# Performance work log

Measured on AMD Instinct MI355X. Metric: run time of the kernel, lower is better.

The kernel has to match this reference:

```python
import jax, jax.numpy as jnp
import numpy as np

EPS = 1e-5
H, W, D_FULL, D_RFFT, DIM = 9, 11, 9, 5, 900  # spectral grid 9x11x9, rfft last dim -> 5

def layer_norm(x, gamma, beta):
    mu = jnp.mean(x, axis=-1, keepdims=True)
    var = jnp.var(x, axis=-1, keepdims=True)
    return (x - mu) * jax.lax.rsqrt(var + EPS) * gamma + beta

def setup_inputs() -> dict:
    key = jax.random.key(0)
    ks = jax.random.split(key, 12)
    B, N, C = 64, H * W * D_FULL, DIM  # N = 891
    hidden, rank = int(C * 2.0), C // 2  # 1800, 450
    return {
        "x": jax.random.normal(ks[0], (B, N, C), dtype=jnp.float32),
        # Global_Filter complex weight: (h, w, d, dim, 2), init ~ N(0,1)*0.02
        "cw": jax.random.normal(ks[1], (H, W, D_RFFT, C, 2), dtype=jnp.float32) * 0.02,
        "gamma1": jnp.ones((C,), jnp.float32),
        "beta1": jnp.zeros((C,), jnp.float32),
        "gamma2": jnp.ones((C,), jnp.float32),
        "beta2": jnp.zeros((C,), jnp.float32),
        # low-rank MLP (torch Linear weights are (out, in); we apply x @ W.T)
        "u1_w": jax.random.normal(ks[2], (rank, C), jnp.float32) * (1.0 / np.sqrt(C)),
        "v1_w": jax.random.normal(ks[3], (hidden, rank), jnp.float32) * (1.0 / np.sqrt(rank)),
        "v1_b": jnp.zeros((hidden,), jnp.float32),
        "u2_w": jax.random.normal(ks[4], (rank, hidden), jnp.float32) * (1.0 / np.sqrt(hidden)),
        "v2_w": jax.random.normal(ks[5], (C, rank), jnp.float32) * (1.0 / np.sqrt(rank)),
        "v2_b": jnp.zeros((C,), jnp.float32),
    }

def reference(x, cw, gamma1, beta1, gamma2, beta2, u1_w, v1_w, v1_b, u2_w, v2_w, v2_b):
    B, N, C = x.shape
    # norm1 -> global spectral filter
    y = layer_norm(x, gamma1, beta1)
    y = y.reshape(B, H, W, D_FULL, C)
    yf = jnp.fft.rfftn(y, axes=(1, 2, 3), norm="ortho")  # (B, 9, 11, 5, C) complex
    weight = jax.lax.complex(cw[..., 0], cw[..., 1])      # (9, 11, 5, C)
    yf = yf * weight
    y = jnp.fft.irfftn(yf, s=(H, W, D_FULL), axes=(1, 2, 3), norm="ortho")
    y = y.reshape(B, N, C)
    # norm2 -> low-rank MLP (dropout/droppath = identity in eval)
    z = layer_norm(y, gamma2, beta2)
    z = jnp.einsum("bnc,rc->bnr", z, u1_w)
    z = jnp.einsum("bnr,hr->bnh", z, v1_w) + v1_b
    z = jax.nn.gelu(z, approximate=False)
    z = jnp.einsum("bnh,rh->bnr", z, u2_w)
    z = jnp.einsum("bnr,cr->bnc", z, v2_w) + v2_b
    return x + z
```

## Files before the change

### kernel.cpp

```cpp
#include <hip/hip_runtime.h>


typedef unsigned short u16;
typedef __bf16 bf16x8 __attribute__((ext_vector_type(8)));
typedef float f32x4 __attribute__((ext_vector_type(4)));

#define LN_EPS 1e-5f
#define CH 16

constexpr float KC9[9] = {
  1.0f, 0.766044443118978f, 0.17364817766693041f, -0.4999999999999998f,
  -0.9396926207859083f, -0.9396926207859084f, -0.5000000000000004f,
  0.17364817766692997f, 0.7660444431189778f };
constexpr float KS9[9] = {
  0.0f, 0.6427876096865393f, 0.984807753012208f, 0.8660254037844387f,
  0.3420201433256689f, -0.34202014332566866f, -0.8660254037844385f,
  -0.9848077530122081f, -0.6427876096865396f };
constexpr float KC11[11] = {
  1.0f, 0.8412535328311812f, 0.41541501300188644f, -0.14231483827328512f,
  -0.654860733945285f, -0.9594929736144974f, -0.9594929736144974f,
  -0.6548607339452852f, -0.14231483827328543f, 0.4154150130018863f,
  0.8412535328311811f };
constexpr float KS11[11] = {
  0.0f, 0.5406408174555976f, 0.9096319953545183f, 0.9898214418809327f,
  0.7557495743542583f, 0.2817325568414297f, -0.2817325568414296f,
  -0.7557495743542582f, -0.9898214418809327f, -0.9096319953545184f,
  -0.5406408174555979f };

__device__ __forceinline__ u16 f2bf(float f) {
  unsigned int u = __float_as_uint(f);
  return (u16)((u + 0x7fffu + ((u >> 16) & 1u)) >> 16);
}
__device__ __forceinline__ float gelu_f(float v) {
  float t = 0.7978845608028654f * v * (1.f + 0.044715f * v * v);
  float e = __expf(2.f * t);
  float th = 1.f - 2.f * __builtin_amdgcn_rcpf(e + 1.f);
  return 0.5f * v * (1.f + th);
}

__global__ __launch_bounds__(256) void k_cvt(const float* __restrict__ s, u16* __restrict__ d,
                                             int rows, int sc, int dc,
                                             const float* __restrict__ gamma) {
  int i = blockIdx.x * 256 + threadIdx.x;
  if (i >= rows * dc) return;
  int r = i / dc, c = i % dc;
  u16 o = 0;
  if (c < sc) {
    float v = s[(size_t)r * sc + c];
    if (gamma) v *= gamma[c];
    o = f2bf(v);
  }
  d[i] = o;
}

__global__ __launch_bounds__(256) void k_bias1(const float* __restrict__ u1w,
                                               const float* __restrict__ b2,
                                               float* __restrict__ out) {
  int r = blockIdx.x * 256 + threadIdx.x;
  if (r < 450) {
    float s = 0.f;
    for (int c = 0; c < 900; c++) s += u1w[r * 900 + c] * b2[c];
    out[r] = s;
  }
}

__global__ __launch_bounds__(256) void k_stats1(const float* __restrict__ x,
                                                float2* __restrict__ stats) {
  int tok = blockIdx.x * 4 + (threadIdx.x >> 6);
  int l = threadIdx.x & 63;
  const float* row = x + (size_t)tok * 900;
  float s1 = 0.f, s2 = 0.f;
#pragma unroll
  for (int j = 0; j < 15; j++) {
    int c = l + j * 64;
    if (c < 900) { float a = row[c]; s1 += a; s2 += a * a; }
  }
#pragma unroll
  for (int off = 32; off; off >>= 1) { s1 += __shfl_xor(s1, off, 64); s2 += __shfl_xor(s2, off, 64); }
  if (l == 0) {
    float m = s1 * (1.f / 900.f);
    float var = s2 * (1.f / 900.f) - m * m;
    stats[tok] = make_float2(m, rsqrtf(var + LN_EPS));
  }
}

__global__ __launch_bounds__(256) void k_spectral(const float* __restrict__ x,
                                                  const float2* __restrict__ stats,
                                                  const float* __restrict__ g1,
                                                  const float* __restrict__ b1,
                                                  const float* __restrict__ cw,
                                                  float* __restrict__ y) {
  __shared__ float sre[5 * 99 * CH];
  __shared__ float sim[5 * 99 * CH];
  int b = blockIdx.x / 57, cc = blockIdx.x % 57;
  int c0 = cc * CH;
  int t = threadIdx.x;
  const float* xb = x + (size_t)b * 801900;
  const float2* st = stats + (size_t)b * 891;

  for (int col = t; col < 99 * CH; col += 256) {
    int pos = col / CH, c = col % CH;
    int cg = c0 + c; bool ok = cg < 900;
    float g = ok ? g1[cg] : 0.f, be = ok ? b1[cg] : 0.f;
    float yv[9];
#pragma unroll
    for (int d = 0; d < 9; d++) {
      float a = ok ? xb[(size_t)(pos * 9 + d) * 900 + cg] : 0.f;
      float2 s = st[pos * 9 + d];
      yv[d] = (a - s.x) * s.y * g + be;
    }
#pragma unroll
    for (int kd = 0; kd < 5; kd++) {
      float re = 0.f, im = 0.f;
#pragma unroll
      for (int d = 0; d < 9; d++) { int j = (kd * d) % 9; re += yv[d] * KC9[j]; im -= yv[d] * KS9[j]; }
      sre[(kd * 99 + pos) * CH + c] = re;
      sim[(kd * 99 + pos) * CH + c] = im;
    }
  }
  __syncthreads();

  for (int col = t; col < 5 * 9 * CH; col += 256) {
    int kd = col / (9 * CH), r = col % (9 * CH), h = r / CH, c = r % CH;
    int base = (kd * 99 + h * 11) * CH + c;
    float xr[11], xi[11];
#pragma unroll
    for (int w = 0; w < 11; w++) { xr[w] = sre[base + w * CH]; xi[w] = sim[base + w * CH]; }
#pragma unroll
    for (int k = 0; k < 11; k++) {
      float yr = 0.f, yi = 0.f;
#pragma unroll
      for (int w = 0; w < 11; w++) {
        int j = (k * w) % 11; float cf = KC11[j], sf = KS11[j];
        yr += xr[w] * cf + xi[w] * sf;
        yi += xi[w] * cf - xr[w] * sf;
      }
      sre[base + k * CH] = yr; sim[base + k * CH] = yi;
    }
  }
  __syncthreads();

  for (int col = t; col < 5 * 11 * CH; col += 256) {
    int kd = col / (11 * CH), r = col % (11 * CH), kw = r / CH, c = r % CH;
    int cg = c0 + c;
    int base = (kd * 99 + kw) * CH + c;
    float xr[9], xi[9];
#pragma unroll
    for (int h = 0; h < 9; h++) { xr[h] = sre[base + h * 11 * CH]; xi[h] = sim[base + h * 11 * CH]; }
    float zr[9], zi[9];
#pragma unroll
    for (int k = 0; k < 9; k++) {
      float yr = 0.f, yi = 0.f;
#pragma unroll
      for (int h = 0; h < 9; h++) {
        int j = (k * h) % 9; float cf = KC9[j], sf = KS9[j];
        yr += xr[h] * cf + xi[h] * sf;
        yi += xi[h] * cf - xr[h] * sf;
      }
      float wr = 0.f, wi = 0.f;
      if (cg < 900) {
        size_t widx = ((size_t)((k * 11 + kw) * 5 + kd) * 900 + cg) * 2;
        wr = cw[widx]; wi = cw[widx + 1];
      }
      zr[k] = yr * wr - yi * wi;
      zi[k] = yr * wi + yi * wr;
    }
#pragma unroll
    for (int h = 0; h < 9; h++) {
      float orr = 0.f, oi = 0.f;
#pragma unroll
      for (int k = 0; k < 9; k++) {
        int j = (k * h) % 9; float cf = KC9[j], sf = KS9[j];
        orr += zr[k] * cf - zi[k] * sf;
        oi  += zi[k] * cf + zr[k] * sf;
      }
      sre[base + h * 11 * CH] = orr; sim[base + h * 11 * CH] = oi;
    }
  }
  __syncthreads();

  for (int col = t; col < 5 * 9 * CH; col += 256) {
    int kd = col / (9 * CH), r = col % (9 * CH), h = r / CH, c = r % CH;
    int base = (kd * 99 + h * 11) * CH + c;
    float xr[11], xi[11];
#pragma unroll
    for (int w = 0; w < 11; w++) { xr[w] = sre[base + w * CH]; xi[w] = sim[base + w * CH]; }
#pragma unroll
    for (int k = 0; k < 11; k++) {
      float yr = 0.f, yi = 0.f;
#pragma unroll
      for (int w = 0; w < 11; w++) {
        int j = (k * w) % 11; float cf = KC11[j], sf = KS11[j];
        yr += xr[w] * cf - xi[w] * sf;
        yi += xi[w] * cf + xr[w] * sf;
      }
      sre[base + k * CH] = yr; sim[base + k * CH] = yi;
    }
  }
  __syncthreads();

  for (int col = t; col < 99 * CH; col += 256) {
    int pos = col / CH, c = col % CH;
    int cg = c0 + c;
    if (cg >= 900) continue;
    float Xr[5], Xi[5];
#pragma unroll
    for (int k = 0; k < 5; k++) { Xr[k] = sre[(k * 99 + pos) * CH + c]; Xi[k] = sim[(k * 99 + pos) * CH + c]; }
#pragma unroll
    for (int d = 0; d < 9; d++) {
      float acc = Xr[0];
#pragma unroll
      for (int k = 1; k < 5; k++) { int j = (k * d) % 9; acc += 2.f * (Xr[k] * KC9[j] - Xi[k] * KS9[j]); }
      y[((size_t)b * 891 + pos * 9 + d) * 900 + cg] = acc * (1.f / 891.f);
    }
  }
}

__global__ __launch_bounds__(256) void k_ln2(const float* __restrict__ y, u16* __restrict__ yn) {
  int tok = blockIdx.x * 4 + (threadIdx.x >> 6);
  int l = threadIdx.x & 63;
  const float* row = y + (size_t)tok * 900;
  float v[15];
  float s1 = 0.f, s2 = 0.f;
#pragma unroll
  for (int j = 0; j < 15; j++) {
    int c = l + j * 64;
    float a = (c < 900) ? row[c] : 0.f;
    v[j] = a; s1 += a; s2 += a * a;
  }
#pragma unroll
  for (int off = 32; off; off >>= 1) { s1 += __shfl_xor(s1, off, 64); s2 += __shfl_xor(s2, off, 64); }
  float m = s1 * (1.f / 900.f);
  float var = s2 * (1.f / 900.f) - m * m;
  float rs = rsqrtf(var + LN_EPS);
  u16* orow = yn + (size_t)tok * 928;
#pragma unroll
  for (int j = 0; j < 15; j++) {
    int c = l + j * 64;
    if (c < 900) orow[c] = f2bf((v[j] - m) * rs);
    else if (c < 928) orow[c] = 0;
  }
}

typedef __attribute__((address_space(1))) void gvoid;
typedef __attribute__((address_space(3))) void svoid;

__device__ __forceinline__ void stage16(const u16* g, u16* lbase, int lane) {
#if __has_builtin(__builtin_amdgcn_global_load_lds)
  __builtin_amdgcn_global_load_lds((gvoid*)(void*)g, (svoid*)lbase, 16, 0, 0);
#else
  *(uint4*)(lbase + lane * 8) = *(const uint4*)g;
#endif
}

template <int EPI>
__global__ __launch_bounds__(256, 2) void k_gemm(
    const u16* __restrict__ A, const u16* __restrict__ B,
    int M, int N, int Kt, int ldk, int NT,
    u16* __restrict__ Ob, int ldo, int Nstore,
    const float* __restrict__ bias,
    const float* __restrict__ Xres, float* __restrict__ Of) {
  __shared__ u16 As[128 * 32];
  __shared__ u16 Bs[128 * 32];
  int t = threadIdx.x, w = t >> 6, l = t & 63;
  int mt = blockIdx.x / NT, nt = blockIdx.x % NT;
  int m0 = mt * 128, n0 = nt * 128;
  int arow = (w << 4) + (l >> 2);
  int koff = (l & 3) * 8;
  int wm = (w >> 1) << 6, wn = (w & 1) << 6;
  int fr = l & 15, fq = l >> 4;

  f32x4 acc[4][4];
  f32x4 zero = {0.f, 0.f, 0.f, 0.f};
#pragma unroll
  for (int i = 0; i < 4; i++)
#pragma unroll
    for (int j = 0; j < 4; j++) acc[i][j] = zero;

  for (int kt = 0; kt < Kt; ++kt) {
    int k0 = kt * 32;
#pragma unroll
    for (int j = 0; j < 2; j++) {
      int r = (j << 6) + arow;
      int gm = m0 + r; gm = gm < M ? gm : M - 1;
      stage16(A + (size_t)gm * ldk + (k0 + koff), &As[((j << 6) + (w << 4)) * 32], l);
      int gn = n0 + r; gn = gn < N ? gn : N - 1;
      stage16(B + (size_t)gn * ldk + (k0 + koff), &Bs[((j << 6) + (w << 4)) * 32], l);
    }
    __syncthreads();
    bf16x8 af[4], bfr[4];
#pragma unroll
    for (int i = 0; i < 4; i++) af[i] = *(const bf16x8*)&As[(wm + (i << 4) + fr) * 32 + fq * 8];
#pragma unroll
    for (int i = 0; i < 4; i++) bfr[i] = *(const bf16x8*)&Bs[(wn + (i << 4) + fr) * 32 + fq * 8];
#pragma unroll
    for (int i = 0; i < 4; i++)
#pragma unroll
      for (int j = 0; j < 4; j++)
        acc[i][j] = __builtin_amdgcn_mfma_f32_16x16x32_bf16(af[i], bfr[j], acc[i][j], 0, 0, 0);
    __syncthreads();
  }

#pragma unroll
  for (int j = 0; j < 4; j++) {
    int gn = n0 + wn + (j << 4) + fr;
    float bv = 0.f;
    if (EPI != 2) bv = (gn < Nstore) ? bias[gn] : 0.f;
#pragma unroll
    for (int i = 0; i < 4; i++) {
#pragma unroll
      for (int r = 0; r < 4; r++) {
        int gm = m0 + wm + (i << 4) + (fq << 2) + r;
        if (gm < M) {
          float val = acc[i][j][r] + bv;
          if (EPI == 1) val = gelu_f(val);
          if (EPI == 3) {
            if (gn < Nstore) Of[(size_t)gm * Nstore + gn] = val + Xres[(size_t)gm * Nstore + gn];
          } else {
            if (gn < ldo) Ob[(size_t)gm * ldo + gn] = (gn < Nstore) ? f2bf(val) : (u16)0;
          }
        }
      }
    }
  }
}

extern "C" void kernel_launch(void* const* d_in, const int* in_sizes, int n_in,
                              void* d_out, int out_size, void* d_ws, size_t ws_size,
                              hipStream_t stream) {
  const float* x   = (const float*)d_in[0];
  const float* cw  = (const float*)d_in[1];
  const float* g1  = (const float*)d_in[2];
  const float* b1  = (const float*)d_in[3];
  const float* g2  = (const float*)d_in[4];
  const float* b2  = (const float*)d_in[5];
  const float* u1w = (const float*)d_in[6];
  const float* v1w = (const float*)d_in[7];
  const float* v1b = (const float*)d_in[8];
  const float* u2w = (const float*)d_in[9];
  const float* v2w = (const float*)d_in[10];
  const float* v2b = (const float*)d_in[11];

  char* ws = (char*)d_ws;
  float* y   = (float*)ws;
  u16*   t2  = (u16*)ws;
  u16*   t3  = (u16*)(ws + 228096000);
  u16*   u1g = (u16*)(ws + 286488576);
  u16*   v1c = (u16*)(ws + 287323776);
  u16*   u2c = (u16*)(ws + 289166976);
  u16*   v2c = (u16*)(ws + 290808576);
  float* b1r = (float*)(ws + 291730176);

  u16*    yn    = (u16*)d_out;
  u16*    t1    = (u16*)((char*)d_out + 105836544);
  float2* stats = (float2*)((char*)d_out + 164229120);
  float*  outF  = (float*)d_out;

  k_cvt<<<1632, 256, 0, stream>>>(u1w, u1g, 450, 900, 928, g2);
  k_cvt<<<3600, 256, 0, stream>>>(v1w, v1c, 1800, 450, 512, nullptr);
  k_cvt<<<3207, 256, 0, stream>>>(u2w, u2c, 450, 1800, 1824, nullptr);
  k_cvt<<<1800, 256, 0, stream>>>(v2w, v2c, 900, 450, 512, nullptr);
  k_bias1<<<2, 256, 0, stream>>>(u1w, b2, b1r);

  k_stats1<<<14256, 256, 0, stream>>>(x, stats);
  k_spectral<<<64 * 57, 256, 0, stream>>>(x, stats, g1, b1, cw, y);
  k_ln2<<<14256, 256, 0, stream>>>(y, yn);

  k_gemm<0><<<446 * 4,  256, 0, stream>>>(yn, u1g, 57024, 450,  29, 928,  4,  t1, 512, 450, b1r, nullptr, nullptr);
  k_gemm<1><<<446 * 15, 256, 0, stream>>>(t1, v1c, 57024, 1800, 16, 512,  15, t2, 1824, 1800, v1b, nullptr, nullptr);
  k_gemm<2><<<446 * 4,  256, 0, stream>>>(t2, u2c, 57024, 450,  57, 1824, 4,  t3, 512, 450, nullptr, nullptr, nullptr);
  k_gemm<3><<<446 * 8,  256, 0, stream>>>(t3, v2c, 57024, 900,  16, 512,  8,  nullptr, 0, 900, v2b, x, outF);
}
```

Measured before the change: 1.496 ms.

## Double-buffer GEMM LDS tiles with prefetch two k-steps ahead

Measured after the change: 1.491 ms. About the same (-0.3%).

```diff
diff --git a/kernel.cpp b/kernel.cpp
--- a/kernel.cpp
+++ b/kernel.cpp
@@ -245,12 +245,23 @@
 typedef __attribute__((address_space(1))) void gvoid;
 typedef __attribute__((address_space(3))) void svoid;
 
-__device__ __forceinline__ void stage16(const u16* g, u16* lbase, int lane) {
-#if __has_builtin(__builtin_amdgcn_global_load_lds)
+__device__ __forceinline__ void stage16(const u16* g, u16* lbase) {
   __builtin_amdgcn_global_load_lds((gvoid*)(void*)g, (svoid*)lbase, 16, 0, 0);
-#else
-  *(uint4*)(lbase + lane * 8) = *(const uint4*)g;
-#endif
+}
+
+__device__ __forceinline__ void stage_tile(const u16* __restrict__ A, const u16* __restrict__ B,
+                                           int m0, int n0, int M, int N, int ldk, int k0,
+                                           u16* As, u16* Bs, int w, int l) {
+  int arow = (w << 4) + (l >> 2);
+  int koff = k0 + (l & 3) * 8;
+#pragma unroll
+  for (int j = 0; j < 2; j++) {
+    int r = (j << 6) + arow;
+    int gm = m0 + r; gm = gm < M ? gm : M - 1;
+    stage16(A + (size_t)gm * ldk + koff, &As[((j << 6) + (w << 4)) * 32]);
+    int gn = n0 + r; gn = gn < N ? gn : N - 1;
+    stage16(B + (size_t)gn * ldk + koff, &Bs[((j << 6) + (w << 4)) * 32]);
+  }
 }
 
 template <int EPI>
@@ -260,13 +271,11 @@
     u16* __restrict__ Ob, int ldo, int Nstore,
     const float* __restrict__ bias,
     const float* __restrict__ Xres, float* __restrict__ Of) {
-  __shared__ u16 As[128 * 32];
-  __shared__ u16 Bs[128 * 32];
+  __shared__ u16 As[2][128 * 32];
+  __shared__ u16 Bs[2][128 * 32];
   int t = threadIdx.x, w = t >> 6, l = t & 63;
   int mt = blockIdx.x / NT, nt = blockIdx.x % NT;
   int m0 = mt * 128, n0 = nt * 128;
-  int arow = (w << 4) + (l >> 2);
-  int koff = (l & 3) * 8;
   int wm = (w >> 1) << 6, wn = (w & 1) << 6;
   int fr = l & 15, fq = l >> 4;
 
@@ -277,28 +286,29 @@
 #pragma unroll
     for (int j = 0; j < 4; j++) acc[i][j] = zero;
 
+  stage_tile(A, B, m0, n0, M, N, ldk, 0, As[0], Bs[0], w, l);
+  if (Kt > 1) stage_tile(A, B, m0, n0, M, N, ldk, 32, As[1], Bs[1], w, l);
+
   for (int kt = 0; kt < Kt; ++kt) {
-    int k0 = kt * 32;
-#pragma unroll
-    for (int j = 0; j < 2; j++) {
-      int r = (j << 6) + arow;
-      int gm = m0 + r; gm = gm < M ? gm : M - 1;
-      stage16(A + (size_t)gm * ldk + (k0 + koff), &As[((j << 6) + (w << 4)) * 32], l);
-      int gn = n0 + r; gn = gn < N ? gn : N - 1;
-      stage16(B + (size_t)gn * ldk + (k0 + koff), &Bs[((j << 6) + (w << 4)) * 32], l);
-    }
-    __syncthreads();
+    if (kt + 1 < Kt) asm volatile("s_waitcnt vmcnt(4)\n\ts_barrier" ::: "memory");
+    else             asm volatile("s_waitcnt vmcnt(0)\n\ts_barrier" ::: "memory");
+
+    const u16* as = As[kt & 1];
+    const u16* bs = Bs[kt & 1];
     bf16x8 af[4], bfr[4];
 #pragma unroll
-    for (int i = 0; i < 4; i++) af[i] = *(const bf16x8*)&As[(wm + (i << 4) + fr) * 32 + fq * 8];
-#pragma unroll
-    for (int i = 0; i < 4; i++) bfr[i] = *(const bf16x8*)&Bs[(wn + (i << 4) + fr) * 32 + fq * 8];
+    for (int i = 0; i < 4; i++) af[i] = *(const bf16x8*)&as[(wm + (i << 4) + fr) * 32 + fq * 8];
+#pragma unroll
+    for (int i = 0; i < 4; i++) bfr[i] = *(const bf16x8*)&bs[(wn + (i << 4) + fr) * 32 + fq * 8];
 #pragma unroll
     for (int i = 0; i < 4; i++)
 #pragma unroll
       for (int j = 0; j < 4; j++)
         acc[i][j] = __builtin_amdgcn_mfma_f32_16x16x32_bf16(af[i], bfr[j], acc[i][j], 0, 0, 0);
-    __syncthreads();
+
+    asm volatile("s_barrier" ::: "memory");
+    if (kt + 2 < Kt)
+      stage_tile(A, B, m0, n0, M, N, ldk, (kt + 2) * 32, As[kt & 1], Bs[kt & 1], w, l);
   }
 
 #pragma unroll
```
